# Kernel optimization log

Measured on AMD Instinct MI355X. Metric: run time of the kernel, lower is better.

The kernel has to match this reference:

```python
import jax, jax.numpy as jnp
import numpy as np

N_QUBITS = 4
N_LAYERS = 2
FS = 2          # filter_size
STRIDE = 1
DIM = 2 ** N_QUBITS  # 16

# mean over qubits of PauliZ eigenvalue per computational-basis state
_idx = np.arange(DIM)
_bits = np.stack([(_idx >> (N_QUBITS - 1 - q)) & 1 for q in range(N_QUBITS)], 0)  # [4,16]
Z_MEAN = jnp.asarray((1.0 - 2.0 * _bits).mean(0), dtype=jnp.float32)               # [16]


def ry_mat(t):
    c, s = jnp.cos(t / 2), jnp.sin(t / 2)
    m = jnp.stack([jnp.stack([c, -s], -1), jnp.stack([s, c], -1)], -2)
    return m.astype(jnp.complex64)


def rx_mat(t):
    c = jnp.cos(t / 2).astype(jnp.complex64)
    s = (jnp.sin(t / 2) * (-1j)).astype(jnp.complex64)
    return jnp.stack([jnp.stack([c, s], -1), jnp.stack([s, c], -1)], -2)


def rz_mat(t):
    e = jnp.exp((t / 2).astype(jnp.complex64) * (-1j))
    z = jnp.zeros_like(e)
    return jnp.stack([jnp.stack([e, z], -1), jnp.stack([z, jnp.conj(e)], -1)], -2)


def apply_1q(state, U, q):
    # state: [N,2,2,2,2] complex; U: [2,2] or batched [N,2,2]
    st = jnp.moveaxis(state, 1 + q, -1)
    if U.ndim == 3:
        st = jnp.einsum('nab,n...b->n...a', U, st)
    else:
        st = jnp.einsum('ab,n...b->n...a', U, st)
    return jnp.moveaxis(st, -1, 1 + q)


def apply_cnot(state, c, t):
    st = jnp.moveaxis(state, (1 + c, 1 + t), (-2, -1))
    st = jnp.stack([st[..., 0, :], st[..., 1, ::-1]], axis=-2)
    return jnp.moveaxis(st, (-2, -1), (1 + c, 1 + t))


def apply_cry(state, theta, c, t):
    U = ry_mat(theta)
    st = jnp.moveaxis(state, (1 + c, 1 + t), (-2, -1))
    bot = jnp.einsum('ab,n...b->n...a', U, st[..., 1, :])
    st = jnp.stack([st[..., 0, :], bot], axis=-2)
    return jnp.moveaxis(st, (-2, -1), (1 + c, 1 + t))


def _forward(x, weights):
    B, H, W, C = x.shape
    oh = (H - FS) // STRIDE + 1
    ow = (W - FS) // STRIDE + 1
    # extract all patches at once: [B, oh, ow, FS, FS, C]
    ri = (jnp.arange(oh) * STRIDE)[:, None, None, None] + jnp.arange(FS)[None, None, :, None]
    ci = (jnp.arange(ow) * STRIDE)[None, :, None, None] + jnp.arange(FS)[None, None, None, :]
    patches = x[:, ri, ci, :]
    pf = patches.reshape(B * oh * ow, FS * FS * C)
    # tf.nn.l2_normalize over the whole (flat) patch, eps=1e-12
    norm = pf * jax.lax.rsqrt(jnp.maximum(jnp.sum(pf * pf, -1, keepdims=True), 1e-12))
    ang = norm[:, :N_QUBITS]  # RY angles, [N,4]
    N = pf.shape[0]

    # |0000> encoded state, batched over all patches
    state = jnp.zeros((N, DIM), jnp.complex64).at[:, 0].set(1.0)
    state = state.reshape((N,) + (2,) * N_QUBITS)
    for q in range(N_QUBITS):
        state = apply_1q(state, ry_mat(ang[:, q]), q)
    for q in range(N_QUBITS - 1):
        state = apply_cnot(state, q, q + 1)

    outs = []
    for f in range(weights.shape[0]):
        w = weights[f]
        s = state
        for layer in range(N_LAYERS):
            base = layer * N_QUBITS * 3
            for q in range(N_QUBITS):
                p = base + q * 3
                s = apply_1q(s, rx_mat(w[p]), q)
                s = apply_1q(s, ry_mat(w[p + 1]), q)
                s = apply_1q(s, rz_mat(w[p + 2]), q)
            # CRY on even pairs, reusing weights[base + i] (as in the source)
            for q in range(0, N_QUBITS - 1, 2):
                s = apply_cry(s, w[base + q], q, q + 1)
        sf = s.reshape(N, DIM)
        probs = jnp.real(sf * jnp.conj(sf))           # [N,16]
        outs.append((probs @ Z_MEAN).reshape(B, oh, ow))  # mean of <Z_q>
    return jnp.stack(outs, -1)  # [B, oh, ow, n_filters]


def setup_inputs() -> dict:
    key = jax.random.key(0)
    k1, k2 = jax.random.split(key)
    x = jax.random.normal(k1, (8, 96, 96, 16), dtype=jnp.float32)
    # keras 'random_uniform' initializer default range
    weights = jax.random.uniform(k2, (8, 24), dtype=jnp.float32, minval=-0.05, maxval=0.05)
    return {"x": x, "weights": weights}


def reference(x, weights):
    return _forward(x, weights)
```

## Files before the change

kernel.cpp:

```cpp
#include <hip/hip_runtime.h>

namespace {
constexpr int DIM = 16;
constexpr int BATCH = 8;
constexpr int H = 96, W = 96, CH = 16;
constexpr int OH = 95, OW = 95;
constexpr int NF = 8, NW = 24;
constexpr int NPIX = BATCH * OH * OW;
}

__global__ __launch_bounds__(256)
void qconv_kernel(const float* __restrict__ x, const float* __restrict__ wts,
                  float* __restrict__ out) {
  __shared__ float lc[NF * NW];
  __shared__ float ls[NF * NW];
  const int tid = threadIdx.x;
  if (tid < NF * NW) {
    const float h = wts[tid] * 0.5f;
    float s, c;
    __sincosf(h, &s, &c);
    lc[tid] = c;
    ls[tid] = s;
  }
  __syncthreads();

  const int n = blockIdx.x * 256 + tid;
  if (n >= NPIX) return;
  const int b = n / (OH * OW);
  const int rem = n - b * (OH * OW);
  const int oi = rem / OW;
  const int oj = rem - oi * OW;

  const float* base = x + (((b * H) + oi) * W + oj) * CH;
  float sumsq = 0.f;
  float4 f0 = make_float4(0.f, 0.f, 0.f, 0.f);
#pragma unroll
  for (int fi = 0; fi < 2; ++fi) {
    const float4* row = reinterpret_cast<const float4*>(base + fi * W * CH);
#pragma unroll
    for (int k = 0; k < 8; ++k) {
      const float4 v = row[k];
      if (fi == 0 && k == 0) f0 = v;
      sumsq = fmaf(v.x, v.x, sumsq);
      sumsq = fmaf(v.y, v.y, sumsq);
      sumsq = fmaf(v.z, v.z, sumsq);
      sumsq = fmaf(v.w, v.w, sumsq);
    }
  }
  const float inv = rsqrtf(fmaxf(sumsq, 1e-12f));

  float cq[4], sq[4];
  __sincosf(f0.x * inv * 0.5f, &sq[0], &cq[0]);
  __sincosf(f0.y * inv * 0.5f, &sq[1], &cq[1]);
  __sincosf(f0.z * inv * 0.5f, &sq[2], &cq[2]);
  __sincosf(f0.w * inv * 0.5f, &sq[3], &cq[3]);

  float init[DIM];
#pragma unroll
  for (int i = 0; i < DIM; ++i) {
    init[i] = ((i & 8) ? sq[0] : cq[0]) * ((i & 4) ? sq[1] : cq[1]) *
              ((i & 2) ? sq[2] : cq[2]) * ((i & 1) ? sq[3] : cq[3]);
  }
#pragma unroll
  for (int i = 0; i < DIM; ++i)
    if ((i & 8) && !(i & 4)) { const float t = init[i]; init[i] = init[i | 4]; init[i | 4] = t; }
#pragma unroll
  for (int i = 0; i < DIM; ++i)
    if ((i & 4) && !(i & 2)) { const float t = init[i]; init[i] = init[i | 2]; init[i | 2] = t; }
#pragma unroll
  for (int i = 0; i < DIM; ++i)
    if ((i & 2) && !(i & 1)) { const float t = init[i]; init[i] = init[i | 1]; init[i | 1] = t; }

  float* op = out + n * NF;
  for (int f = 0; f < NF; ++f) {
    const float* fc = lc + f * NW;
    const float* fs = ls + f * NW;
    float ar[DIM], ai[DIM];
#pragma unroll
    for (int i = 0; i < DIM; ++i) { ar[i] = init[i]; ai[i] = 0.f; }

#pragma unroll
    for (int layer = 0; layer < 2; ++layer) {
      const int wb = layer * 12;
#pragma unroll
      for (int q = 0; q < 4; ++q) {
        const int m = 8 >> q;
        {
          const float c = fc[wb + q * 3], s = fs[wb + q * 3];
#pragma unroll
          for (int i = 0; i < DIM; ++i) {
            if (i & m) continue;
            const int j = i | m;
            const float a0r = ar[i], a0i = ai[i], a1r = ar[j], a1i = ai[j];
            ar[i] = fmaf(c, a0r,  s * a1i);
            ai[i] = fmaf(c, a0i, -s * a1r);
            ar[j] = fmaf(c, a1r,  s * a0i);
            ai[j] = fmaf(c, a1i, -s * a0r);
          }
        }
        {
          const float c = fc[wb + q * 3 + 1], s = fs[wb + q * 3 + 1];
#pragma unroll
          for (int i = 0; i < DIM; ++i) {
            if (i & m) continue;
            const int j = i | m;
            const float a0r = ar[i], a0i = ai[i], a1r = ar[j], a1i = ai[j];
            ar[i] = fmaf(c, a0r, -s * a1r);
            ai[i] = fmaf(c, a0i, -s * a1i);
            ar[j] = fmaf(s, a0r,  c * a1r);
            ai[j] = fmaf(s, a0i,  c * a1i);
          }
        }
        {
          const float c = fc[wb + q * 3 + 2], s = fs[wb + q * 3 + 2];
#pragma unroll
          for (int i = 0; i < DIM; ++i) {
            const float r = ar[i], im = ai[i];
            if (i & m) {
              ar[i] = fmaf(c, r, -s * im);
              ai[i] = fmaf(c, im,  s * r);
            } else {
              ar[i] = fmaf(c, r,   s * im);
              ai[i] = fmaf(c, im, -s * r);
            }
          }
        }
      }
      {
        const float c = fc[wb + 0], s = fs[wb + 0];
#pragma unroll
        for (int i = 0; i < DIM; ++i) {
          if (!(i & 8) || (i & 4)) continue;
          const int j = i | 4;
          const float a0r = ar[i], a0i = ai[i], a1r = ar[j], a1i = ai[j];
          ar[i] = fmaf(c, a0r, -s * a1r);
          ai[i] = fmaf(c, a0i, -s * a1i);
          ar[j] = fmaf(s, a0r,  c * a1r);
          ai[j] = fmaf(s, a0i,  c * a1i);
        }
      }
      {
        const float c = fc[wb + 2], s = fs[wb + 2];
#pragma unroll
        for (int i = 0; i < DIM; ++i) {
          if (!(i & 2) || (i & 1)) continue;
          const int j = i | 1;
          const float a0r = ar[i], a0i = ai[i], a1r = ar[j], a1i = ai[j];
          ar[i] = fmaf(c, a0r, -s * a1r);
          ai[i] = fmaf(c, a0i, -s * a1i);
          ar[j] = fmaf(s, a0r,  c * a1r);
          ai[j] = fmaf(s, a0i,  c * a1i);
        }
      }
    }

    float p[DIM];
#pragma unroll
    for (int i = 0; i < DIM; ++i) p[i] = fmaf(ar[i], ar[i], ai[i] * ai[i]);
    const float acc = (p[0] - p[15]) +
                      0.5f * ((p[1] + p[2] + p[4] + p[8]) -
                              (p[7] + p[11] + p[13] + p[14]));
    op[f] = acc;
  }
}

extern "C" void kernel_launch(void* const* d_in, const int* in_sizes, int n_in,
                              void* d_out, int out_size, void* d_ws, size_t ws_size,
                              hipStream_t stream) {
  const float* x = (const float*)d_in[0];
  const float* w = (const float*)d_in[1];
  float* out = (float*)d_out;
  const int nblocks = (NPIX + 255) / 256;
  qconv_kernel<<<dim3(nblocks), dim3(256), 0, stream>>>(x, w, out);
}
```

Before: 85.93 us.

## Assign one thread per (pixel, filter) pair with shuffle-reduced patch norm

Each pixel's 8 filters move from a serial loop in one thread to 8 separate threads, so the kernel launches 8x more threads. The 64-float patch load for the L2 norm is split across the 8 lanes and combined with xor-shuffles. The trig tables are transposed to [weight][filter] so lanes reading the same weight index hit consecutive shared-memory words, and the output store becomes fully coalesced. In exchange, each lane recomputes the initial state encoding and an extra wave-level reduction is added.

```diff
diff --git a/kernel.cpp b/kernel.cpp
--- a/kernel.cpp
+++ b/kernel.cpp
@@ -7,47 +7,52 @@
 constexpr int OH = 95, OW = 95;
 constexpr int NF = 8, NW = 24;
 constexpr int NPIX = BATCH * OH * OW;
+constexpr int NTHREAD = NPIX * NF;
 }
 
 __global__ __launch_bounds__(256)
 void qconv_kernel(const float* __restrict__ x, const float* __restrict__ wts,
                   float* __restrict__ out) {
-  __shared__ float lc[NF * NW];
-  __shared__ float ls[NF * NW];
+  __shared__ float lc[NW * NF];
+  __shared__ float ls[NW * NF];
   const int tid = threadIdx.x;
   if (tid < NF * NW) {
+    const int f = tid / NW;
+    const int k = tid - f * NW;
     const float h = wts[tid] * 0.5f;
     float s, c;
     __sincosf(h, &s, &c);
-    lc[tid] = c;
-    ls[tid] = s;
+    lc[k * NF + f] = c;
+    ls[k * NF + f] = s;
   }
   __syncthreads();
 
-  const int n = blockIdx.x * 256 + tid;
+  const int t = blockIdx.x * 256 + tid;
+  const int n = t >> 3;
+  const int f = t & 7;
   if (n >= NPIX) return;
+
   const int b = n / (OH * OW);
   const int rem = n - b * (OH * OW);
   const int oi = rem / OW;
   const int oj = rem - oi * OW;
 
   const float* base = x + (((b * H) + oi) * W + oj) * CH;
-  float sumsq = 0.f;
-  float4 f0 = make_float4(0.f, 0.f, 0.f, 0.f);
-#pragma unroll
-  for (int fi = 0; fi < 2; ++fi) {
-    const float4* row = reinterpret_cast<const float4*>(base + fi * W * CH);
-#pragma unroll
-    for (int k = 0; k < 8; ++k) {
-      const float4 v = row[k];
-      if (fi == 0 && k == 0) f0 = v;
-      sumsq = fmaf(v.x, v.x, sumsq);
-      sumsq = fmaf(v.y, v.y, sumsq);
-      sumsq = fmaf(v.z, v.z, sumsq);
-      sumsq = fmaf(v.w, v.w, sumsq);
-    }
-  }
-  const float inv = rsqrtf(fmaxf(sumsq, 1e-12f));
+  const float4* lp = reinterpret_cast<const float4*>(
+      base + (f >> 2) * W * CH + (f & 3) * 8);
+  const float4 v0 = lp[0];
+  const float4 v1 = lp[1];
+  float ss = 0.f;
+  ss = fmaf(v0.x, v0.x, ss); ss = fmaf(v0.y, v0.y, ss);
+  ss = fmaf(v0.z, v0.z, ss); ss = fmaf(v0.w, v0.w, ss);
+  ss = fmaf(v1.x, v1.x, ss); ss = fmaf(v1.y, v1.y, ss);
+  ss = fmaf(v1.z, v1.z, ss); ss = fmaf(v1.w, v1.w, ss);
+  ss += __shfl_xor(ss, 1);
+  ss += __shfl_xor(ss, 2);
+  ss += __shfl_xor(ss, 4);
+  const float inv = rsqrtf(fmaxf(ss, 1e-12f));
+
+  const float4 f0 = *reinterpret_cast<const float4*>(base);
 
   float cq[4], sq[4];
   __sincosf(f0.x * inv * 0.5f, &sq[0], &cq[0]);
@@ -55,83 +60,51 @@
   __sincosf(f0.z * inv * 0.5f, &sq[2], &cq[2]);
   __sincosf(f0.w * inv * 0.5f, &sq[3], &cq[3]);
 
-  float init[DIM];
+  float ar[DIM], ai[DIM];
 #pragma unroll
   for (int i = 0; i < DIM; ++i) {
-    init[i] = ((i & 8) ? sq[0] : cq[0]) * ((i & 4) ? sq[1] : cq[1]) *
-              ((i & 2) ? sq[2] : cq[2]) * ((i & 1) ? sq[3] : cq[3]);
+    ar[i] = ((i & 8) ? sq[0] : cq[0]) * ((i & 4) ? sq[1] : cq[1]) *
+            ((i & 2) ? sq[2] : cq[2]) * ((i & 1) ? sq[3] : cq[3]);
+    ai[i] = 0.f;
   }
 #pragma unroll
   for (int i = 0; i < DIM; ++i)
-    if ((i & 8) && !(i & 4)) { const float t = init[i]; init[i] = init[i | 4]; init[i | 4] = t; }
+    if ((i & 8) && !(i & 4)) { const float tt = ar[i]; ar[i] = ar[i | 4]; ar[i | 4] = tt; }
 #pragma unroll
   for (int i = 0; i < DIM; ++i)
-    if ((i & 4) && !(i & 2)) { const float t = init[i]; init[i] = init[i | 2]; init[i | 2] = t; }
+    if ((i & 4) && !(i & 2)) { const float tt = ar[i]; ar[i] = ar[i | 2]; ar[i | 2] = tt; }
 #pragma unroll
   for (int i = 0; i < DIM; ++i)
-    if ((i & 2) && !(i & 1)) { const float t = init[i]; init[i] = init[i | 1]; init[i | 1] = t; }
+    if ((i & 2) && !(i & 1)) { const float tt = ar[i]; ar[i] = ar[i | 1]; ar[i | 1] = tt; }
 
-  float* op = out + n * NF;
-  for (int f = 0; f < NF; ++f) {
-    const float* fc = lc + f * NW;
-    const float* fs = ls + f * NW;
-    float ar[DIM], ai[DIM];
-#pragma unroll
-    for (int i = 0; i < DIM; ++i) { ar[i] = init[i]; ai[i] = 0.f; }
+#define FC(k) lc[(k) * NF + f]
+#define FS_(k) ls[(k) * NF + f]
 
 #pragma unroll
-    for (int layer = 0; layer < 2; ++layer) {
-      const int wb = layer * 12;
+  for (int layer = 0; layer < 2; ++layer) {
+    const int wb = layer * 12;
 #pragma unroll
-      for (int q = 0; q < 4; ++q) {
-        const int m = 8 >> q;
-        {
-          const float c = fc[wb + q * 3], s = fs[wb + q * 3];
+    for (int q = 0; q < 4; ++q) {
+      const int m = 8 >> q;
+      {
+        const float c = FC(wb + q * 3), s = FS_(wb + q * 3);
 #pragma unroll
-          for (int i = 0; i < DIM; ++i) {
-            if (i & m) continue;
-            const int j = i | m;
-            const float a0r = ar[i], a0i = ai[i], a1r = ar[j], a1i = ai[j];
-            ar[i] = fmaf(c, a0r,  s * a1i);
-            ai[i] = fmaf(c, a0i, -s * a1r);
-            ar[j] = fmaf(c, a1r,  s * a0i);
-            ai[j] = fmaf(c, a1i, -s * a0r);
-          }
-        }
-        {
-          const float c = fc[wb + q * 3 + 1], s = fs[wb + q * 3 + 1];
-#pragma unroll
-          for (int i = 0; i < DIM; ++i) {
-            if (i & m) continue;
-            const int j = i | m;
-            const float a0r = ar[i], a0i = ai[i], a1r = ar[j], a1i = ai[j];
-            ar[i] = fmaf(c, a0r, -s * a1r);
-            ai[i] = fmaf(c, a0i, -s * a1i);
-            ar[j] = fmaf(s, a0r,  c * a1r);
-            ai[j] = fmaf(s, a0i,  c * a1i);
-          }
-        }
-        {
-          const float c = fc[wb + q * 3 + 2], s = fs[wb + q * 3 + 2];
-#pragma unroll
-          for (int i = 0; i < DIM; ++i) {
-            const float r = ar[i], im = ai[i];
-            if (i & m) {
-              ar[i] = fmaf(c, r, -s * im);
-              ai[i] = fmaf(c, im,  s * r);
-            } else {
-              ar[i] = fmaf(c, r,   s * im);
-              ai[i] = fmaf(c, im, -s * r);
-            }
-          }
+        for (int i = 0; i < DIM; ++i) {
+          if (i & m) continue;
+          const int j = i | m;
+          const float a0r = ar[i], a0i = ai[i], a1r = ar[j], a1i = ai[j];
+          ar[i] = fmaf(c, a0r,  s * a1i);
+          ai[i] = fmaf(c, a0i, -s * a1r);
+          ar[j] = fmaf(c, a1r,  s * a0i);
+          ai[j] = fmaf(c, a1i, -s * a0r);
         }
       }
       {
-        const float c = fc[wb + 0], s = fs[wb + 0];
+        const float c = FC(wb + q * 3 + 1), s = FS_(wb + q * 3 + 1);
 #pragma unroll
         for (int i = 0; i < DIM; ++i) {
-          if (!(i & 8) || (i & 4)) continue;
-          const int j = i | 4;
+          if (i & m) continue;
+          const int j = i | m;
           const float a0r = ar[i], a0i = ai[i], a1r = ar[j], a1i = ai[j];
           ar[i] = fmaf(c, a0r, -s * a1r);
           ai[i] = fmaf(c, a0i, -s * a1i);
@@ -140,28 +113,57 @@
         }
       }
       {
-        const float c = fc[wb + 2], s = fs[wb + 2];
+        const float c = FC(wb + q * 3 + 2), s = FS_(wb + q * 3 + 2);
 #pragma unroll
         for (int i = 0; i < DIM; ++i) {
-          if (!(i & 2) || (i & 1)) continue;
-          const int j = i | 1;
-          const float a0r = ar[i], a0i = ai[i], a1r = ar[j], a1i = ai[j];
-          ar[i] = fmaf(c, a0r, -s * a1r);
-          ai[i] = fmaf(c, a0i, -s * a1i);
-          ar[j] = fmaf(s, a0r,  c * a1r);
-          ai[j] = fmaf(s, a0i,  c * a1i);
+          const float r = ar[i], im = ai[i];
+          if (i & m) {
+            ar[i] = fmaf(c, r, -s * im);
+            ai[i] = fmaf(c, im,  s * r);
+          } else {
+            ar[i] = fmaf(c, r,   s * im);
+            ai[i] = fmaf(c, im, -s * r);
+          }
         }
       }
     }
+    {
+      const float c = FC(wb + 0), s = FS_(wb + 0);
+#pragma unroll
+      for (int i = 0; i < DIM; ++i) {
+        if (!(i & 8) || (i & 4)) continue;
+        const int j = i | 4;
+        const float a0r = ar[i], a0i = ai[i], a1r = ar[j], a1i = ai[j];
+        ar[i] = fmaf(c, a0r, -s * a1r);
+        ai[i] = fmaf(c, a0i, -s * a1i);
+        ar[j] = fmaf(s, a0r,  c * a1r);
+        ai[j] = fmaf(s, a0i,  c * a1i);
+      }
+    }
+    {
+      const float c = FC(wb + 2), s = FS_(wb + 2);
+#pragma unroll
+      for (int i = 0; i < DIM; ++i) {
+        if (!(i & 2) || (i & 1)) continue;
+        const int j = i | 1;
+        const float a0r = ar[i], a0i = ai[i], a1r = ar[j], a1i = ai[j];
+        ar[i] = fmaf(c, a0r, -s * a1r);
+        ai[i] = fmaf(c, a0i, -s * a1i);
+        ar[j] = fmaf(s, a0r,  c * a1r);
+        ai[j] = fmaf(s, a0i,  c * a1i);
+      }
+    }
+  }
+#undef FC
+#undef FS_
 
-    float p[DIM];
+  float p[DIM];
 #pragma unroll
-    for (int i = 0; i < DIM; ++i) p[i] = fmaf(ar[i], ar[i], ai[i] * ai[i]);
-    const float acc = (p[0] - p[15]) +
-                      0.5f * ((p[1] + p[2] + p[4] + p[8]) -
-                              (p[7] + p[11] + p[13] + p[14]));
-    op[f] = acc;
-  }
+  for (int i = 0; i < DIM; ++i) p[i] = fmaf(ar[i], ar[i], ai[i] * ai[i]);
+  const float acc = (p[0] - p[15]) +
+                    0.5f * ((p[1] + p[2] + p[4] + p[8]) -
+                            (p[7] + p[11] + p[13] + p[14]));
+  out[t] = acc;
 }
 
 extern "C" void kernel_launch(void* const* d_in, const int* in_sizes, int n_in,
@@ -170,6 +172,6 @@
   const float* x = (const float*)d_in[0];
   const float* w = (const float*)d_in[1];
   float* out = (float*)d_out;
-  const int nblocks = (NPIX + 255) / 256;
+  const int nblocks = (NTHREAD + 255) / 256;
   qconv_kernel<<<dim3(nblocks), dim3(256), 0, stream>>>(x, w, out);
 }
```

Result: faster. 76.97 us (-10.4%).

## Precompute per-filter 16x16 circuit unitaries and apply as real-input matvec

Applied to the files above, without the earlier changes.

Instead of simulating all gates per pixel per filter, a small kernel builds each filter's full 16x16 complex unitary once from the weights. A second kernel computes each pixel's initial real state vector into workspace, and a third kernel applies the unitary via shared-memory matvec per (pixel, filter). This replaces many per-pixel gate ops with 512 FMAs per pixel-filter, at the cost of three launches and a round trip of state vectors through global memory.

```diff
diff --git a/kernel.cpp b/kernel.cpp
--- a/kernel.cpp
+++ b/kernel.cpp
@@ -7,131 +7,45 @@
 constexpr int OH = 95, OW = 95;
 constexpr int NF = 8, NW = 24;
 constexpr int NPIX = BATCH * OH * OW;
-}
-
-__global__ __launch_bounds__(256)
-void qconv_kernel(const float* __restrict__ x, const float* __restrict__ wts,
-                  float* __restrict__ out) {
-  __shared__ float lc[NF * NW];
-  __shared__ float ls[NF * NW];
-  const int tid = threadIdx.x;
-  if (tid < NF * NW) {
-    const float h = wts[tid] * 0.5f;
-    float s, c;
-    __sincosf(h, &s, &c);
-    lc[tid] = c;
-    ls[tid] = s;
-  }
-  __syncthreads();
-
-  const int n = blockIdx.x * 256 + tid;
-  if (n >= NPIX) return;
-  const int b = n / (OH * OW);
-  const int rem = n - b * (OH * OW);
-  const int oi = rem / OW;
-  const int oj = rem - oi * OW;
-
-  const float* base = x + (((b * H) + oi) * W + oj) * CH;
-  float sumsq = 0.f;
-  float4 f0 = make_float4(0.f, 0.f, 0.f, 0.f);
-#pragma unroll
-  for (int fi = 0; fi < 2; ++fi) {
-    const float4* row = reinterpret_cast<const float4*>(base + fi * W * CH);
-#pragma unroll
-    for (int k = 0; k < 8; ++k) {
-      const float4 v = row[k];
-      if (fi == 0 && k == 0) f0 = v;
-      sumsq = fmaf(v.x, v.x, sumsq);
-      sumsq = fmaf(v.y, v.y, sumsq);
-      sumsq = fmaf(v.z, v.z, sumsq);
-      sumsq = fmaf(v.w, v.w, sumsq);
-    }
-  }
-  const float inv = rsqrtf(fmaxf(sumsq, 1e-12f));
-
-  float cq[4], sq[4];
-  __sincosf(f0.x * inv * 0.5f, &sq[0], &cq[0]);
-  __sincosf(f0.y * inv * 0.5f, &sq[1], &cq[1]);
-  __sincosf(f0.z * inv * 0.5f, &sq[2], &cq[2]);
-  __sincosf(f0.w * inv * 0.5f, &sq[3], &cq[3]);
-
-  float init[DIM];
-#pragma unroll
-  for (int i = 0; i < DIM; ++i) {
-    init[i] = ((i & 8) ? sq[0] : cq[0]) * ((i & 4) ? sq[1] : cq[1]) *
-              ((i & 2) ? sq[2] : cq[2]) * ((i & 1) ? sq[3] : cq[3]);
-  }
-#pragma unroll
-  for (int i = 0; i < DIM; ++i)
-    if ((i & 8) && !(i & 4)) { const float t = init[i]; init[i] = init[i | 4]; init[i | 4] = t; }
-#pragma unroll
-  for (int i = 0; i < DIM; ++i)
-    if ((i & 4) && !(i & 2)) { const float t = init[i]; init[i] = init[i | 2]; init[i | 2] = t; }
-#pragma unroll
-  for (int i = 0; i < DIM; ++i)
-    if ((i & 2) && !(i & 1)) { const float t = init[i]; init[i] = init[i | 1]; init[i | 1] = t; }
-
-  float* op = out + n * NF;
-  for (int f = 0; f < NF; ++f) {
-    const float* fc = lc + f * NW;
-    const float* fs = ls + f * NW;
-    float ar[DIM], ai[DIM];
-#pragma unroll
-    for (int i = 0; i < DIM; ++i) { ar[i] = init[i]; ai[i] = 0.f; }
-
-#pragma unroll
-    for (int layer = 0; layer < 2; ++layer) {
-      const int wb = layer * 12;
-#pragma unroll
-      for (int q = 0; q < 4; ++q) {
-        const int m = 8 >> q;
-        {
-          const float c = fc[wb + q * 3], s = fs[wb + q * 3];
-#pragma unroll
-          for (int i = 0; i < DIM; ++i) {
-            if (i & m) continue;
-            const int j = i | m;
-            const float a0r = ar[i], a0i = ai[i], a1r = ar[j], a1i = ai[j];
-            ar[i] = fmaf(c, a0r,  s * a1i);
-            ai[i] = fmaf(c, a0i, -s * a1r);
-            ar[j] = fmaf(c, a1r,  s * a0i);
-            ai[j] = fmaf(c, a1i, -s * a0r);
-          }
+constexpr int PBLK = (NPIX + 255) / 256;
+constexpr int PSI_OFF = NF * 512;
+}
+
+__global__ void build_u_kernel(const float* __restrict__ wts, float* __restrict__ ws) {
+  const int f = blockIdx.x;
+  const int col = threadIdx.x;
+  const float* w = wts + f * NW;
+
+  float ar[DIM], ai[DIM];
+#pragma unroll
+  for (int i = 0; i < DIM; ++i) { ar[i] = (i == col) ? 1.f : 0.f; ai[i] = 0.f; }
+
+#pragma unroll
+  for (int layer = 0; layer < 2; ++layer) {
+    const int wb = layer * 12;
+#pragma unroll
+    for (int q = 0; q < 4; ++q) {
+      const int m = 8 >> q;
+      float c, s;
+      {
+        __sincosf(w[wb + q * 3] * 0.5f, &s, &c);
+#pragma unroll
+        for (int i = 0; i < DIM; ++i) {
+          if (i & m) continue;
+          const int j = i | m;
+          const float a0r = ar[i], a0i = ai[i], a1r = ar[j], a1i = ai[j];
+          ar[i] = fmaf(c, a0r,  s * a1i);
+          ai[i] = fmaf(c, a0i, -s * a1r);
+          ar[j] = fmaf(c, a1r,  s * a0i);
+          ai[j] = fmaf(c, a1i, -s * a0r);
         }
-        {
-          const float c = fc[wb + q * 3 + 1], s = fs[wb + q * 3 + 1];
-#pragma unroll
-          for (int i = 0; i < DIM; ++i) {
-            if (i & m) continue;
-            const int j = i | m;
-            const float a0r = ar[i], a0i = ai[i], a1r = ar[j], a1i = ai[j];
-            ar[i] = fmaf(c, a0r, -s * a1r);
-            ai[i] = fmaf(c, a0i, -s * a1i);
-            ar[j] = fmaf(s, a0r,  c * a1r);
-            ai[j] = fmaf(s, a0i,  c * a1i);
-          }
-        }
-        {
-          const float c = fc[wb + q * 3 + 2], s = fs[wb + q * 3 + 2];
-#pragma unroll
-          for (int i = 0; i < DIM; ++i) {
-            const float r = ar[i], im = ai[i];
-            if (i & m) {
-              ar[i] = fmaf(c, r, -s * im);
-              ai[i] = fmaf(c, im,  s * r);
-            } else {
-              ar[i] = fmaf(c, r,   s * im);
-              ai[i] = fmaf(c, im, -s * r);
-            }
-          }
-        }
       }
       {
-        const float c = fc[wb + 0], s = fs[wb + 0];
+        __sincosf(w[wb + q * 3 + 1] * 0.5f, &s, &c);
 #pragma unroll
         for (int i = 0; i < DIM; ++i) {
-          if (!(i & 8) || (i & 4)) continue;
-          const int j = i | 4;
+          if (i & m) continue;
+          const int j = i | m;
           const float a0r = ar[i], a0i = ai[i], a1r = ar[j], a1i = ai[j];
           ar[i] = fmaf(c, a0r, -s * a1r);
           ai[i] = fmaf(c, a0i, -s * a1i);
@@ -140,28 +54,153 @@
         }
       }
       {
-        const float c = fc[wb + 2], s = fs[wb + 2];
+        __sincosf(w[wb + q * 3 + 2] * 0.5f, &s, &c);
 #pragma unroll
         for (int i = 0; i < DIM; ++i) {
-          if (!(i & 2) || (i & 1)) continue;
-          const int j = i | 1;
-          const float a0r = ar[i], a0i = ai[i], a1r = ar[j], a1i = ai[j];
-          ar[i] = fmaf(c, a0r, -s * a1r);
-          ai[i] = fmaf(c, a0i, -s * a1i);
-          ar[j] = fmaf(s, a0r,  c * a1r);
-          ai[j] = fmaf(s, a0i,  c * a1i);
+          const float r = ar[i], im = ai[i];
+          if (i & m) { ar[i] = fmaf(c, r, -s * im); ai[i] = fmaf(c, im,  s * r); }
+          else       { ar[i] = fmaf(c, r,  s * im); ai[i] = fmaf(c, im, -s * r); }
         }
       }
     }
-
-    float p[DIM];
-#pragma unroll
-    for (int i = 0; i < DIM; ++i) p[i] = fmaf(ar[i], ar[i], ai[i] * ai[i]);
-    const float acc = (p[0] - p[15]) +
-                      0.5f * ((p[1] + p[2] + p[4] + p[8]) -
-                              (p[7] + p[11] + p[13] + p[14]));
-    op[f] = acc;
-  }
+    {
+      float c, s;
+      __sincosf(w[wb + 0] * 0.5f, &s, &c);
+#pragma unroll
+      for (int i = 0; i < DIM; ++i) {
+        if (!(i & 8) || (i & 4)) continue;
+        const int j = i | 4;
+        const float a0r = ar[i], a0i = ai[i], a1r = ar[j], a1i = ai[j];
+        ar[i] = fmaf(c, a0r, -s * a1r);
+        ai[i] = fmaf(c, a0i, -s * a1i);
+        ar[j] = fmaf(s, a0r,  c * a1r);
+        ai[j] = fmaf(s, a0i,  c * a1i);
+      }
+    }
+    {
+      float c, s;
+      __sincosf(w[wb + 2] * 0.5f, &s, &c);
+#pragma unroll
+      for (int i = 0; i < DIM; ++i) {
+        if (!(i & 2) || (i & 1)) continue;
+        const int j = i | 1;
+        const float a0r = ar[i], a0i = ai[i], a1r = ar[j], a1i = ai[j];
+        ar[i] = fmaf(c, a0r, -s * a1r);
+        ai[i] = fmaf(c, a0i, -s * a1i);
+        ar[j] = fmaf(s, a0r,  c * a1r);
+        ai[j] = fmaf(s, a0i,  c * a1i);
+      }
+    }
+  }
+
+  float* dst = ws + f * 512 + col * 32;
+#pragma unroll
+  for (int i = 0; i < DIM; ++i) { dst[i] = ar[i]; dst[16 + i] = ai[i]; }
+}
+
+__global__ __launch_bounds__(256)
+void psi_kernel(const float* __restrict__ x, float* __restrict__ ws) {
+  const int n = blockIdx.x * 256 + threadIdx.x;
+  if (n >= NPIX) return;
+  const int b = n / (OH * OW);
+  const int rem = n - b * (OH * OW);
+  const int oi = rem / OW;
+  const int oj = rem - oi * OW;
+
+  const float* base = x + (((b * H) + oi) * W + oj) * CH;
+  float ss = 0.f;
+  float4 f0 = make_float4(0.f, 0.f, 0.f, 0.f);
+#pragma unroll
+  for (int fi = 0; fi < 2; ++fi) {
+    const float4* row = reinterpret_cast<const float4*>(base + fi * W * CH);
+#pragma unroll
+    for (int k = 0; k < 8; ++k) {
+      const float4 v = row[k];
+      if (fi == 0 && k == 0) f0 = v;
+      ss = fmaf(v.x, v.x, ss); ss = fmaf(v.y, v.y, ss);
+      ss = fmaf(v.z, v.z, ss); ss = fmaf(v.w, v.w, ss);
+    }
+  }
+  const float inv = rsqrtf(fmaxf(ss, 1e-12f));
+
+  float cq[4], sq[4];
+  __sincosf(f0.x * inv * 0.5f, &sq[0], &cq[0]);
+  __sincosf(f0.y * inv * 0.5f, &sq[1], &cq[1]);
+  __sincosf(f0.z * inv * 0.5f, &sq[2], &cq[2]);
+  __sincosf(f0.w * inv * 0.5f, &sq[3], &cq[3]);
+
+  float st[DIM];
+#pragma unroll
+  for (int i = 0; i < DIM; ++i) {
+    const float pr = ((i & 8) ? sq[0] : cq[0]) * ((i & 4) ? sq[1] : cq[1]) *
+                     ((i & 2) ? sq[2] : cq[2]) * ((i & 1) ? sq[3] : cq[3]);
+    int j = i;
+    if (j & 8) j ^= 4;
+    if (j & 4) j ^= 2;
+    if (j & 2) j ^= 1;
+    st[j] = pr;
+  }
+
+  float4* dst = reinterpret_cast<float4*>(ws + PSI_OFF + n * 16);
+  dst[0] = make_float4(st[0], st[1], st[2], st[3]);
+  dst[1] = make_float4(st[4], st[5], st[6], st[7]);
+  dst[2] = make_float4(st[8], st[9], st[10], st[11]);
+  dst[3] = make_float4(st[12], st[13], st[14], st[15]);
+}
+
+__global__ __launch_bounds__(256)
+void apply_kernel(const float* __restrict__ ws, float* __restrict__ out) {
+  __shared__ float U[512];
+  const int tid = threadIdx.x;
+  const int f = blockIdx.y;
+  if (tid < 128)
+    reinterpret_cast<float4*>(U)[tid] =
+        reinterpret_cast<const float4*>(ws + f * 512)[tid];
+  __syncthreads();
+
+  const int n = blockIdx.x * 256 + tid;
+  const bool valid = n < NPIX;
+  const int nc = valid ? n : NPIX - 1;
+
+  float psi[DIM];
+  {
+    const float4* pp = reinterpret_cast<const float4*>(ws + PSI_OFF + nc * 16);
+    const float4 a = pp[0], b4 = pp[1], c4 = pp[2], d4 = pp[3];
+    psi[0] = a.x;  psi[1] = a.y;  psi[2] = a.z;  psi[3] = a.w;
+    psi[4] = b4.x; psi[5] = b4.y; psi[6] = b4.z; psi[7] = b4.w;
+    psi[8] = c4.x; psi[9] = c4.y; psi[10] = c4.z; psi[11] = c4.w;
+    psi[12] = d4.x; psi[13] = d4.y; psi[14] = d4.z; psi[15] = d4.w;
+  }
+
+  float yr[DIM], yi[DIM];
+#pragma unroll
+  for (int i = 0; i < DIM; ++i) { yr[i] = 0.f; yi[i] = 0.f; }
+
+  const float4* l4 = reinterpret_cast<const float4*>(U);
+#define FMA4(dst, d0, v)                      \
+  dst[d0 + 0] = fmaf((v).x, pk, dst[d0 + 0]); \
+  dst[d0 + 1] = fmaf((v).y, pk, dst[d0 + 1]); \
+  dst[d0 + 2] = fmaf((v).z, pk, dst[d0 + 2]); \
+  dst[d0 + 3] = fmaf((v).w, pk, dst[d0 + 3]);
+#pragma unroll
+  for (int k = 0; k < DIM; ++k) {
+    const float pk = psi[k];
+    const float4 r0 = l4[k * 8 + 0], r1 = l4[k * 8 + 1];
+    const float4 r2 = l4[k * 8 + 2], r3 = l4[k * 8 + 3];
+    const float4 i0 = l4[k * 8 + 4], i1 = l4[k * 8 + 5];
+    const float4 i2 = l4[k * 8 + 6], i3 = l4[k * 8 + 7];
+    FMA4(yr, 0, r0) FMA4(yr, 4, r1) FMA4(yr, 8, r2) FMA4(yr, 12, r3)
+    FMA4(yi, 0, i0) FMA4(yi, 4, i1) FMA4(yi, 8, i2) FMA4(yi, 12, i3)
+  }
+#undef FMA4
+
+  float p[DIM];
+#pragma unroll
+  for (int i = 0; i < DIM; ++i) p[i] = fmaf(yr[i], yr[i], yi[i] * yi[i]);
+  const float acc = (p[0] - p[15]) +
+                    0.5f * ((p[1] + p[2] + p[4] + p[8]) -
+                            (p[7] + p[11] + p[13] + p[14]));
+  if (valid) out[nc * NF + f] = acc;
 }
 
 extern "C" void kernel_launch(void* const* d_in, const int* in_sizes, int n_in,
@@ -170,6 +209,9 @@
   const float* x = (const float*)d_in[0];
   const float* w = (const float*)d_in[1];
   float* out = (float*)d_out;
-  const int nblocks = (NPIX + 255) / 256;
-  qconv_kernel<<<dim3(nblocks), dim3(256), 0, stream>>>(x, w, out);
-}
+  float* ws = (float*)d_ws;
+
+  build_u_kernel<<<dim3(NF), dim3(DIM), 0, stream>>>(w, ws);
+  psi_kernel<<<dim3(PBLK), dim3(256), 0, stream>>>(x, ws);
+  apply_kernel<<<dim3(PBLK, NF), dim3(256), 0, stream>>>(ws, out);
+}
```

New measurement: 85.78 us. Within noise of the previous version (-0.2%).

## Precompute per-filter observable matrix and evaluate quadratic form per pixel

Applied to the files above, without the earlier changes.

Rather than simulating the full 4-qubit circuit once per pixel per filter, each block simulates the circuit on the 16 basis states to build the unitary, then forms a real 16x16 observable matrix M = Re(U^H Z U) per filter in shared memory. Each pixel's output becomes the quadratic form psi^T M psi of its real product-state amplitudes, with the CNOT permutation folded into the column index. The block widens to 512 threads split into loader, weight-trig and circuit-simulation roles, and output stores are staged through LDS for coalescing. This trades the per-pixel gate arithmetic for redundant per-block unitary construction, extra LDS traffic and several barriers.

```diff
diff --git a/kernel.cpp b/kernel.cpp
--- a/kernel.cpp
+++ b/kernel.cpp
@@ -2,83 +2,87 @@
 
 namespace {
 constexpr int DIM = 16;
-constexpr int BATCH = 8;
 constexpr int H = 96, W = 96, CH = 16;
 constexpr int OH = 95, OW = 95;
 constexpr int NF = 8, NW = 24;
-constexpr int NPIX = BATCH * OH * OW;
+constexpr int NPIX = 8 * OH * OW;
+constexpr int PPB = 256;
+constexpr int NBLK = (NPIX + PPB - 1) / PPB;
+
+constexpr int OFF_CW = 0;
+constexpr int OFF_SW = 192;
+constexpr int OFF_PSI = 384;
+constexpr int OFF_M = 384 + 4352;
+constexpr int OFF_V = 384 + 4352 + 2048;
+constexpr int VI_REL = 8 * 264;
+constexpr int OFF_OS = OFF_V;
+constexpr int LDS_FLOATS = OFF_V + 2 * 8 * 264;
 }
 
-__global__ __launch_bounds__(256)
-void qconv_kernel(const float* __restrict__ x, const float* __restrict__ wts,
-                  float* __restrict__ out) {
-  __shared__ float lc[NF * NW];
-  __shared__ float ls[NF * NW];
+__global__ __launch_bounds__(512, 4)
+void qconv_one(const float* __restrict__ x, const float* __restrict__ wts,
+               float* __restrict__ out) {
+  __shared__ float sm[LDS_FLOATS];
   const int tid = threadIdx.x;
-  if (tid < NF * NW) {
-    const float h = wts[tid] * 0.5f;
+  const int pbase = blockIdx.x * PPB;
+
+  if (tid >= 256) {
+    int n = pbase + (tid - 256);
+    if (n >= NPIX) n = NPIX - 1;
+    const int b = n / (OH * OW);
+    const int rem = n - b * (OH * OW);
+    const int oi = rem / OW;
+    const int oj = rem - oi * OW;
+
+    const float* base = x + (((b * H) + oi) * W + oj) * CH;
+    float ss = 0.f;
+    float4 f0 = make_float4(0.f, 0.f, 0.f, 0.f);
+#pragma unroll
+    for (int fi = 0; fi < 2; ++fi) {
+      const float4* row = reinterpret_cast<const float4*>(base + fi * W * CH);
+#pragma unroll
+      for (int k = 0; k < 8; ++k) {
+        const float4 v = row[k];
+        if (fi == 0 && k == 0) f0 = v;
+        ss = fmaf(v.x, v.x, ss); ss = fmaf(v.y, v.y, ss);
+        ss = fmaf(v.z, v.z, ss); ss = fmaf(v.w, v.w, ss);
+      }
+    }
+    const float inv = rsqrtf(fmaxf(ss, 1e-12f));
+    float cq[4], sq[4];
+    __sincosf(f0.x * inv * 0.5f, &sq[0], &cq[0]);
+    __sincosf(f0.y * inv * 0.5f, &sq[1], &cq[1]);
+    __sincosf(f0.z * inv * 0.5f, &sq[2], &cq[2]);
+    __sincosf(f0.w * inv * 0.5f, &sq[3], &cq[3]);
+    float* dst = sm + OFF_PSI + (tid - 256) * 17;
+#pragma unroll
+    for (int i = 0; i < DIM; ++i) {
+      dst[i] = ((i & 8) ? sq[0] : cq[0]) * ((i & 4) ? sq[1] : cq[1]) *
+               ((i & 2) ? sq[2] : cq[2]) * ((i & 1) ? sq[3] : cq[3]);
+    }
+  } else if (tid >= 128) {
+    const int i0 = tid - 128;
     float s, c;
-    __sincosf(h, &s, &c);
-    lc[tid] = c;
-    ls[tid] = s;
-  }
-  __syncthreads();
-
-  const int n = blockIdx.x * 256 + tid;
-  if (n >= NPIX) return;
-  const int b = n / (OH * OW);
-  const int rem = n - b * (OH * OW);
-  const int oi = rem / OW;
-  const int oj = rem - oi * OW;
-
-  const float* base = x + (((b * H) + oi) * W + oj) * CH;
-  float sumsq = 0.f;
-  float4 f0 = make_float4(0.f, 0.f, 0.f, 0.f);
-#pragma unroll
-  for (int fi = 0; fi < 2; ++fi) {
-    const float4* row = reinterpret_cast<const float4*>(base + fi * W * CH);
-#pragma unroll
-    for (int k = 0; k < 8; ++k) {
-      const float4 v = row[k];
-      if (fi == 0 && k == 0) f0 = v;
-      sumsq = fmaf(v.x, v.x, sumsq);
-      sumsq = fmaf(v.y, v.y, sumsq);
-      sumsq = fmaf(v.z, v.z, sumsq);
-      sumsq = fmaf(v.w, v.w, sumsq);
-    }
-  }
-  const float inv = rsqrtf(fmaxf(sumsq, 1e-12f));
-
-  float cq[4], sq[4];
-  __sincosf(f0.x * inv * 0.5f, &sq[0], &cq[0]);
-  __sincosf(f0.y * inv * 0.5f, &sq[1], &cq[1]);
-  __sincosf(f0.z * inv * 0.5f, &sq[2], &cq[2]);
-  __sincosf(f0.w * inv * 0.5f, &sq[3], &cq[3]);
-
-  float init[DIM];
-#pragma unroll
-  for (int i = 0; i < DIM; ++i) {
-    init[i] = ((i & 8) ? sq[0] : cq[0]) * ((i & 4) ? sq[1] : cq[1]) *
-              ((i & 2) ? sq[2] : cq[2]) * ((i & 1) ? sq[3] : cq[3]);
-  }
-#pragma unroll
-  for (int i = 0; i < DIM; ++i)
-    if ((i & 8) && !(i & 4)) { const float t = init[i]; init[i] = init[i | 4]; init[i | 4] = t; }
-#pragma unroll
-  for (int i = 0; i < DIM; ++i)
-    if ((i & 4) && !(i & 2)) { const float t = init[i]; init[i] = init[i | 2]; init[i | 2] = t; }
-#pragma unroll
-  for (int i = 0; i < DIM; ++i)
-    if ((i & 2) && !(i & 1)) { const float t = init[i]; init[i] = init[i | 1]; init[i | 1] = t; }
-
-  float* op = out + n * NF;
-  for (int f = 0; f < NF; ++f) {
-    const float* fc = lc + f * NW;
-    const float* fs = ls + f * NW;
+    __sincosf(wts[i0] * 0.5f, &s, &c);
+    sm[OFF_CW + i0] = c;
+    sm[OFF_SW + i0] = s;
+    if (i0 < 64) {
+      const int i1 = i0 + 128;
+      __sincosf(wts[i1] * 0.5f, &s, &c);
+      sm[OFF_CW + i1] = c;
+      sm[OFF_SW + i1] = s;
+    }
+  }
+  __syncthreads();
+
+  if (tid < 128) {
+    const int f = tid >> 4;
+    const int col = tid & 15;
+    const float* fc = sm + OFF_CW + f * NW;
+    const float* fs = sm + OFF_SW + f * NW;
     float ar[DIM], ai[DIM];
 #pragma unroll
-    for (int i = 0; i < DIM; ++i) { ar[i] = init[i]; ai[i] = 0.f; }
-
+    for (int i = 0; i < DIM; ++i) { ar[i] = (i == col) ? 1.f : 0.f; ai[i] = 0.f; }
 #pragma unroll
     for (int layer = 0; layer < 2; ++layer) {
       const int wb = layer * 12;
@@ -116,13 +120,8 @@
 #pragma unroll
           for (int i = 0; i < DIM; ++i) {
             const float r = ar[i], im = ai[i];
-            if (i & m) {
-              ar[i] = fmaf(c, r, -s * im);
-              ai[i] = fmaf(c, im,  s * r);
-            } else {
-              ar[i] = fmaf(c, r,   s * im);
-              ai[i] = fmaf(c, im, -s * r);
-            }
+            if (i & m) { ar[i] = fmaf(c, r, -s * im); ai[i] = fmaf(c, im,  s * r); }
+            else       { ar[i] = fmaf(c, r,  s * im); ai[i] = fmaf(c, im, -s * r); }
           }
         }
       }
@@ -153,14 +152,113 @@
         }
       }
     }
-
-    float p[DIM];
-#pragma unroll
-    for (int i = 0; i < DIM; ++i) p[i] = fmaf(ar[i], ar[i], ai[i] * ai[i]);
-    const float acc = (p[0] - p[15]) +
-                      0.5f * ((p[1] + p[2] + p[4] + p[8]) -
-                              (p[7] + p[11] + p[13] + p[14]));
-    op[f] = acc;
+    const int jc = col ^ (col >> 1);
+    float* vr = sm + OFF_V + f * 264;
+#pragma unroll
+    for (int i = 0; i < DIM; ++i) {
+      vr[i * 16 + jc] = ar[i];
+      vr[VI_REL + i * 16 + jc] = ai[i];
+    }
+  }
+  __syncthreads();
+
+  if (tid < 128) {
+    const int f = tid >> 4;
+    const int tt = tid & 15;
+    const int k0 = (tt >> 2) << 2;
+    const int j0 = (tt & 3) << 2;
+    const float* vr = sm + OFF_V + f * 264;
+    float acc[4][4];
+#pragma unroll
+    for (int a = 0; a < 4; ++a)
+#pragma unroll
+      for (int b2 = 0; b2 < 4; ++b2) acc[a][b2] = 0.f;
+
+#pragma unroll
+    for (int i = 0; i < DIM; ++i) {
+      constexpr float ZT[16] = {1.f, .5f, .5f, 0.f, .5f, 0.f, 0.f, -.5f,
+                                .5f, 0.f, 0.f, -.5f, 0.f, -.5f, -.5f, -1.f};
+      const float z = ZT[i];
+      if (z == 0.f) continue;
+      const float4 kr = *reinterpret_cast<const float4*>(vr + i * 16 + k0);
+      const float4 jr = *reinterpret_cast<const float4*>(vr + i * 16 + j0);
+      const float4 ki = *reinterpret_cast<const float4*>(vr + VI_REL + i * 16 + k0);
+      const float4 ji = *reinterpret_cast<const float4*>(vr + VI_REL + i * 16 + j0);
+      const float zk[4] = {z * kr.x, z * kr.y, z * kr.z, z * kr.w};
+      const float zi[4] = {z * ki.x, z * ki.y, z * ki.z, z * ki.w};
+      const float jrv[4] = {jr.x, jr.y, jr.z, jr.w};
+      const float jiv[4] = {ji.x, ji.y, ji.z, ji.w};
+#pragma unroll
+      for (int a = 0; a < 4; ++a)
+#pragma unroll
+        for (int b2 = 0; b2 < 4; ++b2) {
+          acc[a][b2] = fmaf(zk[a], jrv[b2], acc[a][b2]);
+          acc[a][b2] = fmaf(zi[a], jiv[b2], acc[a][b2]);
+        }
+    }
+    float* mrow = sm + OFF_M + f * 256;
+#pragma unroll
+    for (int a = 0; a < 4; ++a) {
+      *reinterpret_cast<float4*>(mrow + (k0 + a) * 16 + j0) =
+          make_float4(acc[a][0], acc[a][1], acc[a][2], acc[a][3]);
+    }
+  }
+  __syncthreads();
+
+  {
+    const int lane = tid & 63;
+    const int f = __builtin_amdgcn_readfirstlane(tid >> 6);
+    const float* M = sm + OFF_M + f * 256;
+
+    float pa[4][16];
+#pragma unroll
+    for (int p = 0; p < 4; ++p) {
+      const float* ps = sm + OFF_PSI + (p * 64 + lane) * 17;
+#pragma unroll
+      for (int k = 0; k < 16; ++k) pa[p][k] = ps[k];
+    }
+
+    float s[4] = {0.f, 0.f, 0.f, 0.f};
+#pragma unroll
+    for (int k = 0; k < 16; ++k) {
+      const float4 m0 = *reinterpret_cast<const float4*>(M + k * 16 + 0);
+      const float4 m1 = *reinterpret_cast<const float4*>(M + k * 16 + 4);
+      const float4 m2 = *reinterpret_cast<const float4*>(M + k * 16 + 8);
+      const float4 m3 = *reinterpret_cast<const float4*>(M + k * 16 + 12);
+#pragma unroll
+      for (int p = 0; p < 4; ++p) {
+        float rlo = m0.x * pa[p][0];
+        rlo = fmaf(m0.y, pa[p][1], rlo);
+        rlo = fmaf(m0.z, pa[p][2], rlo);
+        rlo = fmaf(m0.w, pa[p][3], rlo);
+        rlo = fmaf(m1.x, pa[p][4], rlo);
+        rlo = fmaf(m1.y, pa[p][5], rlo);
+        rlo = fmaf(m1.z, pa[p][6], rlo);
+        rlo = fmaf(m1.w, pa[p][7], rlo);
+        float rhi = m2.x * pa[p][8];
+        rhi = fmaf(m2.y, pa[p][9], rhi);
+        rhi = fmaf(m2.z, pa[p][10], rhi);
+        rhi = fmaf(m2.w, pa[p][11], rhi);
+        rhi = fmaf(m3.x, pa[p][12], rhi);
+        rhi = fmaf(m3.y, pa[p][13], rhi);
+        rhi = fmaf(m3.z, pa[p][14], rhi);
+        rhi = fmaf(m3.w, pa[p][15], rhi);
+        s[p] = fmaf(pa[p][k], rlo + rhi, s[p]);
+      }
+    }
+#pragma unroll
+    for (int p = 0; p < 4; ++p) sm[OFF_OS + (p * 64 + lane) * 9 + f] = s[p];
+  }
+  __syncthreads();
+
+  {
+    const int pp = tid >> 1;
+    const int e = (tid & 1) * 4;
+    if (tid * 4 < (NPIX - pbase) * 8) {
+      const float* o = sm + OFF_OS + pp * 9 + e;
+      *reinterpret_cast<float4*>(out + (long)pbase * 8 + tid * 4) =
+          make_float4(o[0], o[1], o[2], o[3]);
+    }
   }
 }
 
@@ -170,6 +268,5 @@
   const float* x = (const float*)d_in[0];
   const float* w = (const float*)d_in[1];
   float* out = (float*)d_out;
-  const int nblocks = (NPIX + 255) / 256;
-  qconv_kernel<<<dim3(nblocks), dim3(256), 0, stream>>>(x, w, out);
+  qconv_one<<<dim3(NBLK), dim3(512), 0, stream>>>(x, w, out);
 }
```

Result: faster. 70.74 us (-17.7%).
